# Optimization experiments

Measured on AMD Instinct MI355X. Metric: run time of the kernel, lower is better.

## Reference

```python
import jax, jax.numpy as jnp
import numpy as np

B = 8192
IN = 2048
H = 2048


def setup_inputs() -> dict:
    key = jax.random.key(0)
    ks = jax.random.split(key, 11)
    s_w = 1.0 / np.sqrt(IN + H)  # torch Linear default init scale
    inp = {
        "input": jax.random.normal(ks[0], (B, IN), jnp.float32),
        "h_prev": jax.random.normal(ks[1], (B, H), jnp.float32),
        "c_prev": jax.random.normal(ks[2], (B, H), jnp.float32),
        "Wf": jax.random.normal(ks[3], (H, IN + H), jnp.float32) * s_w,
        "bf": jax.random.normal(ks[4], (H,), jnp.float32) * s_w,
        "Wi": jax.random.normal(ks[5], (H, IN + H), jnp.float32) * s_w,
        "bi": jax.random.normal(ks[6], (H,), jnp.float32) * s_w,
        "Wg": jax.random.normal(ks[7], (H, IN + H), jnp.float32) * s_w,
        "bg": jax.random.normal(ks[8], (H,), jnp.float32) * s_w,
        "Wo": jax.random.normal(ks[9], (H, IN + H), jnp.float32) * s_w,
        "bo": jax.random.normal(ks[10], (H,), jnp.float32) * s_w,
    }
    return inp


def reference(input, h_prev, c_prev, Wf, bf, Wi, bi, Wg, bg, Wo, bo):
    # combined: [B, IN+H]
    combined = jnp.concatenate([input, h_prev], axis=1)
    # Fuse the 4 gate GEMMs into one: W_all [4H, IN+H]
    W_all = jnp.concatenate([Wf, Wi, Wg, Wo], axis=0)
    b_all = jnp.concatenate([bf, bi, bg, bo], axis=0)
    gates = combined @ W_all.T + b_all  # [B, 4H]
    f_, i_, g_, o_ = jnp.split(gates, 4, axis=1)
    f = jax.nn.sigmoid(f_)
    i = jax.nn.sigmoid(i_)
    g = jnp.tanh(g_)
    o = jax.nn.sigmoid(o_)
    c = f * c_prev + i * g
    h = o * jnp.tanh(c)
    return (h, c)
```

## Files before the change

kernel.cpp:

```cpp
#include <hip/hip_runtime.h>
#include <stdint.h>


#define BQ 8192
#define INF 2048
#define HH 2048
#define KK 4096

typedef __attribute__((ext_vector_type(8))) short short8;
typedef __attribute__((ext_vector_type(8))) unsigned short ushort8;
typedef __attribute__((ext_vector_type(4))) float floatx4;

__device__ __forceinline__ unsigned short f2b(float f) {
    unsigned u = __float_as_uint(f);
    u += 0x7fff + ((u >> 16) & 1);
    return (unsigned short)(u >> 16);
}
__device__ __forceinline__ ushort8 cvt8(float4 a, float4 b) {
    ushort8 y;
    y[0] = f2b(a.x); y[1] = f2b(a.y); y[2] = f2b(a.z); y[3] = f2b(a.w);
    y[4] = f2b(b.x); y[5] = f2b(b.y); y[6] = f2b(b.z); y[7] = f2b(b.w);
    return y;
}
__device__ __forceinline__ float fsig(float x) {
    return 1.f / (1.f + __expf(-x));
}
__device__ __forceinline__ float ftanh(float x) {
    return 1.f - 2.f / (__expf(2.f * x) + 1.f);
}

__global__ __launch_bounds__(256) void pack_all(
    const float4* __restrict__ inp, const float4* __restrict__ hp,
    const float4* __restrict__ w0, const float4* __restrict__ w1,
    const float4* __restrict__ w2, const float4* __restrict__ w3,
    unsigned short* __restrict__ comb, unsigned short* __restrict__ wpk)
{
    const int NC16 = BQ * INF / 16;
    int v = blockIdx.x * 256 + threadIdx.x;
    if (v < 2 * NC16) {
        int isH = v >= NC16;
        int u16 = v - (isH ? NC16 : 0);
        const float4* src = isH ? hp : inp;
        float4 x0 = src[u16 * 4];
        float4 x1 = src[u16 * 4 + 1];
        float4 x2 = src[u16 * 4 + 2];
        float4 x3 = src[u16 * 4 + 3];
        int u = u16 * 16;
        int b = u >> 11;
        int k = u & 2047;
        unsigned short* d = comb + (size_t)b * KK + k + (isH ? INF : 0);
        *(ushort8*)d       = cvt8(x0, x1);
        *(ushort8*)(d + 8) = cvt8(x2, x3);
    } else {
        int w = v - 2 * NC16;
        size_t e = (size_t)w * 16;
        int g = (int)(e >> 23);
        int u = (int)(e & ((1u << 23) - 1));
        int h = u >> 12;
        int k = u & 4095;
        const float4* src = (g == 0) ? w0 : (g == 1) ? w1 : (g == 2) ? w2 : w3;
        float4 x0 = src[(u >> 2)];
        float4 x1 = src[(u >> 2) + 1];
        float4 x2 = src[(u >> 2) + 2];
        float4 x3 = src[(u >> 2) + 3];
        int p = ((h >> 5) << 7) + (g << 5) + (h & 31);
        unsigned short* d = wpk + (size_t)p * KK + k;
        *(ushort8*)d       = cvt8(x0, x1);
        *(ushort8*)(d + 8) = cvt8(x2, x3);
    }
}

__global__ __launch_bounds__(512, 2) void lstm_fused(
    const unsigned short* __restrict__ A,
    const unsigned short* __restrict__ W,
    const float* __restrict__ cprev,
    const float* __restrict__ bf_, const float* __restrict__ bi_,
    const float* __restrict__ bg_, const float* __restrict__ bo_,
    float* __restrict__ out)
{
    __shared__ unsigned short lds[65536];
    char* ldsb = (char*)lds;

    const int t    = threadIdx.x;
    const int wv   = t >> 6;
    const int lane = t & 63;
    const int wm   = wv >> 1;
    const int wn   = wv & 1;
    const int fr   = lane & 15;
    const int fq   = lane >> 4;

    int lin = blockIdx.y * 32 + blockIdx.x;
    lin = (lin & 7) * 128 + (lin >> 3);
    const int m0 = (lin >> 5) << 8;
    const int n0 = (lin & 31) << 8;

    const int koff = ((lane & 7) ^ (lane >> 3)) << 3;
    const unsigned short* aR = A + (size_t)(m0 + wv * 16 + (lane >> 3)) * KK + koff;
    const unsigned short* bR = W + (size_t)(n0 + wv * 16 + (lane >> 3)) * KK + koff;
    const int stgOff = wv * 16 * 128;

    const int x7    = fr & 7;
    const int aBase = (wm >> 1) * 16384 + ((wm & 1) * 64 + fr) * 128;
    const int bBase = 32768 + wn * 16384 + fr * 128;

    floatx4 acc[4][8];
#pragma unroll
    for (int i = 0; i < 4; ++i)
#pragma unroll
        for (int j = 0; j < 8; ++j) acc[i][j] = (floatx4)0.f;

    short8 aA[4][2];
    short8 bb[2][2];

#define STAGE(srcbase, ldsoff, kk)                                              \
    do {                                                                        \
        __builtin_amdgcn_global_load_lds(                                       \
            (const __attribute__((address_space(1))) void*)((srcbase) + (kk)),  \
            (__attribute__((address_space(3))) void*)(ldsb + (ldsoff) + stgOff),\
            16, 0, 0);                                                          \
        __builtin_amdgcn_global_load_lds(                                       \
            (const __attribute__((address_space(1))) void*)((srcbase) + 8 * KK + (kk)), \
            (__attribute__((address_space(3))) void*)(ldsb + (ldsoff) + stgOff + 1024), \
            16, 0, 0);                                                          \
    } while (0)

    auto LDA = [&](int side, int i, short8* d) {
        const char* p = ldsb + side * 65536 + aBase + i * 2048;
        d[0] = *(const short8*)(p + ((fq ^ x7) << 4));
        d[1] = *(const short8*)(p + (((4 + fq) ^ x7) << 4));
    };
    auto LDB = [&](int side, int j, short8* d) {
        const char* p = ldsb + side * 65536 + bBase + j * 2048;
        d[0] = *(const short8*)(p + ((fq ^ x7) << 4));
        d[1] = *(const short8*)(p + (((4 + fq) ^ x7) << 4));
    };
    auto MM = [&](const short8* a, const short8* b, floatx4& c) {
        c = __builtin_amdgcn_mfma_f32_16x16x32_bf16(a[0], b[0], c, 0, 0, 0);
        c = __builtin_amdgcn_mfma_f32_16x16x32_bf16(a[1], b[1], c, 0, 0, 0);
    };

#define BAR()  __builtin_amdgcn_s_barrier()
#define SB0()  __builtin_amdgcn_sched_barrier(0)
#define VM4()  do { asm volatile("s_waitcnt vmcnt(4)" ::: "memory"); SB0(); } while (0)

#define CLUSTER(p)                                                    \
    do {                                                              \
        __builtin_amdgcn_s_setprio(1);                                \
        _Pragma("unroll")                                             \
        for (int i = 0; i < 4; ++i) {                                 \
            MM(aA[i], bb[0], acc[i][2 * (p)]);                        \
            MM(aA[i], bb[1], acc[i][2 * (p) + 1]);                    \
        }                                                             \
        __builtin_amdgcn_s_setprio(0);                                \
    } while (0)

    STAGE(aR, 0, 0);
    STAGE(aR + 128 * KK, 16384, 0);
    STAGE(bR, 32768, 0);
    STAGE(bR + 128 * KK, 49152, 0);
    STAGE(aR, 65536, 64);
    STAGE(aR + 128 * KK, 81920, 64);
    VM4();
    BAR();

#pragma unroll 1
    for (int it = 0; it < 32; ++it) {
        const int k1 = ((2 * it + 1) & 63) << 6;
        const int k2 = ((2 * it + 2) & 63) << 6;
        const int k3 = ((2 * it + 3) & 63) << 6;

        LDA(0, 0, aA[0]); LDB(0, 0, bb[0]); LDB(0, 1, bb[1]);
        LDA(0, 1, aA[1]); LDA(0, 2, aA[2]); LDA(0, 3, aA[3]);
        STAGE(bR, 98304, k1);
        SB0();
        CLUSTER(0);
        BAR();

        LDB(0, 2, bb[0]); LDB(0, 3, bb[1]);
        STAGE(bR + 128 * KK, 114688, k1);
        SB0();
        CLUSTER(1);
        BAR();

        LDB(0, 4, bb[0]); LDB(0, 5, bb[1]);
        STAGE(aR, 0, k2);
        SB0();
        CLUSTER(2);
        BAR();

        LDB(0, 6, bb[0]); LDB(0, 7, bb[1]);
        STAGE(aR + 128 * KK, 16384, k2);
        SB0();
        CLUSTER(3);
        VM4();
        BAR();

        LDA(1, 0, aA[0]); LDB(1, 0, bb[0]); LDB(1, 1, bb[1]);
        LDA(1, 1, aA[1]); LDA(1, 2, aA[2]); LDA(1, 3, aA[3]);
        STAGE(bR, 32768, k2);
        SB0();
        CLUSTER(0);
        BAR();

        LDB(1, 2, bb[0]); LDB(1, 3, bb[1]);
        STAGE(bR + 128 * KK, 49152, k2);
        SB0();
        CLUSTER(1);
        BAR();

        LDB(1, 4, bb[0]); LDB(1, 5, bb[1]);
        STAGE(aR, 65536, k3);
        SB0();
        CLUSTER(2);
        BAR();

        LDB(1, 6, bb[0]); LDB(1, 7, bb[1]);
        STAGE(aR + 128 * KK, 81920, k3);
        SB0();
        CLUSTER(3);
        VM4();
        BAR();
    }

    const int hb = (n0 >> 2) + wn * 32;
    float bF[2], bI[2], bG[2], bO[2];
#pragma unroll
    for (int jh = 0; jh < 2; ++jh) {
        int h = hb + jh * 16 + fr;
        bF[jh] = bf_[h]; bI[jh] = bi_[h]; bG[jh] = bg_[h]; bO[jh] = bo_[h];
    }
    const int rowb = m0 + wm * 64 + fq * 4;
#pragma unroll
    for (int i = 0; i < 4; ++i) {
#pragma unroll
        for (int r = 0; r < 4; ++r) {
            int row = rowb + i * 16 + r;
#pragma unroll
            for (int jh = 0; jh < 2; ++jh) {
                int h = hb + jh * 16 + fr;
                size_t gi = (size_t)row * HH + h;
                float xf = acc[i][0 + jh][r] + bF[jh];
                float xi = acc[i][2 + jh][r] + bI[jh];
                float xg = acc[i][4 + jh][r] + bG[jh];
                float xo = acc[i][6 + jh][r] + bO[jh];
                float f  = fsig(xf);
                float ii = fsig(xi);
                float g  = ftanh(xg);
                float o  = fsig(xo);
                float c  = f * cprev[gi] + ii * g;
                float hv = o * ftanh(c);
                out[gi] = hv;
                out[(size_t)BQ * HH + gi] = c;
            }
        }
    }
}

extern "C" void kernel_launch(void* const* d_in, const int* in_sizes, int n_in,
                              void* d_out, int out_size, void* d_ws, size_t ws_size,
                              hipStream_t stream) {
    const float* input  = (const float*)d_in[0];
    const float* h_prev = (const float*)d_in[1];
    const float* c_prev = (const float*)d_in[2];
    const float* Wf = (const float*)d_in[3];
    const float* bf_ = (const float*)d_in[4];
    const float* Wi = (const float*)d_in[5];
    const float* bi_ = (const float*)d_in[6];
    const float* Wg = (const float*)d_in[7];
    const float* bg_ = (const float*)d_in[8];
    const float* Wo = (const float*)d_in[9];
    const float* bo_ = (const float*)d_in[10];
    float* out = (float*)d_out;

    unsigned short* combined = (unsigned short*)d_ws;
    unsigned short* Wpk = (unsigned short*)d_ws + (size_t)BQ * KK;

    pack_all<<<dim3(16384), 256, 0, stream>>>(
        (const float4*)input, (const float4*)h_prev,
        (const float4*)Wf, (const float4*)Wi, (const float4*)Wg, (const float4*)Wo,
        combined, Wpk);
    lstm_fused<<<dim3(32, 32), 512, 0, stream>>>(
        combined, Wpk, c_prev, bf_, bi_, bg_, bo_, out);
}
```

Baseline: 797.1 us.

## Switch to 32x32x16 MFMA tiles and prefetch A/B fragments across phases

Replaces the 16x16x32 bf16 MFMA with 32x32x16 bf16 MFMA, so each wave holds 2x4 floatx16 accumulators instead of 4x8 floatx4. Fewer, larger MFMAs need fewer LDS fragment reads per FLOP. The LDS read schedule is also rebuilt: B fragments are double-buffered in registers (bbA/bbB) and the next A tile is loaded at the end of the previous half-iteration. The vmcnt wait moves earlier and is tightened to vmcnt(2). The epilogue is remapped to the 32x32 output layout, and register pressure changes with the new fragment arrays.

Measured after the change: 2.379 ms. 198% more time.

```diff
diff --git a/kernel.cpp b/kernel.cpp
--- a/kernel.cpp
+++ b/kernel.cpp
@@ -9,7 +9,7 @@
 
 typedef __attribute__((ext_vector_type(8))) short short8;
 typedef __attribute__((ext_vector_type(8))) unsigned short ushort8;
-typedef __attribute__((ext_vector_type(4))) float floatx4;
+typedef __attribute__((ext_vector_type(16))) float floatx16;
 
 __device__ __forceinline__ unsigned short f2b(float f) {
     unsigned u = __float_as_uint(f);
@@ -86,8 +86,9 @@
     const int lane = t & 63;
     const int wm   = wv >> 1;
     const int wn   = wv & 1;
-    const int fr   = lane & 15;
-    const int fq   = lane >> 4;
+    const int lq   = lane & 31;
+    const int lh   = lane >> 5;
+    const int x7   = lq & 7;
 
     int lin = blockIdx.y * 32 + blockIdx.x;
     lin = (lin & 7) * 128 + (lin >> 3);
@@ -99,18 +100,20 @@
     const unsigned short* bR = W + (size_t)(n0 + wv * 16 + (lane >> 3)) * KK + koff;
     const int stgOff = wv * 16 * 128;
 
-    const int x7    = fr & 7;
-    const int aBase = (wm >> 1) * 16384 + ((wm & 1) * 64 + fr) * 128;
-    const int bBase = 32768 + wn * 16384 + fr * 128;
-
-    floatx4 acc[4][8];
-#pragma unroll
-    for (int i = 0; i < 4; ++i)
-#pragma unroll
-        for (int j = 0; j < 8; ++j) acc[i][j] = (floatx4)0.f;
-
-    short8 aA[4][2];
-    short8 bb[2][2];
+    const int aRow = (wm >> 1) * 16384 + (((wm & 1) * 64 + lq) * 128);
+    const int bRow = 32768 + wn * 16384 + lq * 128;
+    int gOff[4];
+#pragma unroll
+    for (int ks = 0; ks < 4; ++ks) gOff[ks] = ((2 * ks + lh) ^ x7) << 4;
+
+    floatx16 acc[2][4];
+#pragma unroll
+    for (int i = 0; i < 2; ++i)
+#pragma unroll
+        for (int g = 0; g < 4; ++g) acc[i][g] = (floatx16)0.f;
+
+    short8 aF[2][4];
+    short8 bbA[4], bbB[4];
 
 #define STAGE(srcbase, ldsoff, kk)                                              \
     do {                                                                        \
@@ -124,34 +127,35 @@
             16, 0, 0);                                                          \
     } while (0)
 
-    auto LDA = [&](int side, int i, short8* d) {
-        const char* p = ldsb + side * 65536 + aBase + i * 2048;
-        d[0] = *(const short8*)(p + ((fq ^ x7) << 4));
-        d[1] = *(const short8*)(p + (((4 + fq) ^ x7) << 4));
+    auto LDAall = [&](int side) {
+#pragma unroll
+        for (int i = 0; i < 2; ++i)
+#pragma unroll
+            for (int ks = 0; ks < 4; ++ks)
+                aF[i][ks] = *(const short8*)(ldsb + side * 65536 + aRow + i * 4096 + gOff[ks]);
     };
-    auto LDB = [&](int side, int j, short8* d) {
-        const char* p = ldsb + side * 65536 + bBase + j * 2048;
-        d[0] = *(const short8*)(p + ((fq ^ x7) << 4));
-        d[1] = *(const short8*)(p + (((4 + fq) ^ x7) << 4));
-    };
-    auto MM = [&](const short8* a, const short8* b, floatx4& c) {
-        c = __builtin_amdgcn_mfma_f32_16x16x32_bf16(a[0], b[0], c, 0, 0, 0);
-        c = __builtin_amdgcn_mfma_f32_16x16x32_bf16(a[1], b[1], c, 0, 0, 0);
+    auto LDB = [&](int side, int g, short8* d) {
+#pragma unroll
+        for (int ks = 0; ks < 4; ++ks)
+            d[ks] = *(const short8*)(ldsb + side * 65536 + bRow + g * 4096 + gOff[ks]);
     };
 
 #define BAR()  __builtin_amdgcn_s_barrier()
 #define SB0()  __builtin_amdgcn_sched_barrier(0)
+#define VM2()  do { asm volatile("s_waitcnt vmcnt(2)" ::: "memory"); SB0(); } while (0)
 #define VM4()  do { asm volatile("s_waitcnt vmcnt(4)" ::: "memory"); SB0(); } while (0)
 
-#define CLUSTER(p)                                                    \
-    do {                                                              \
-        __builtin_amdgcn_s_setprio(1);                                \
-        _Pragma("unroll")                                             \
-        for (int i = 0; i < 4; ++i) {                                 \
-            MM(aA[i], bb[0], acc[i][2 * (p)]);                        \
-            MM(aA[i], bb[1], acc[i][2 * (p) + 1]);                    \
-        }                                                             \
-        __builtin_amdgcn_s_setprio(0);                                \
+#define CL(g, Bb)                                                              \
+    do {                                                                       \
+        __builtin_amdgcn_s_setprio(1);                                         \
+        _Pragma("unroll")                                                      \
+        for (int ks = 0; ks < 4; ++ks) {                                       \
+            acc[0][g] = __builtin_amdgcn_mfma_f32_32x32x16_bf16(               \
+                aF[0][ks], Bb[ks], acc[0][g], 0, 0, 0);                        \
+            acc[1][g] = __builtin_amdgcn_mfma_f32_32x32x16_bf16(               \
+                aF[1][ks], Bb[ks], acc[1][g], 0, 0, 0);                        \
+        }                                                                      \
+        __builtin_amdgcn_s_setprio(0);                                         \
     } while (0)
 
     STAGE(aR, 0, 0);
@@ -162,6 +166,9 @@
     STAGE(aR + 128 * KK, 81920, 64);
     VM4();
     BAR();
+    SB0();
+    LDAall(0);
+    LDB(0, 0, bbA);
 
 #pragma unroll 1
     for (int it = 0; it < 32; ++it) {
@@ -169,89 +176,82 @@
         const int k2 = ((2 * it + 2) & 63) << 6;
         const int k3 = ((2 * it + 3) & 63) << 6;
 
-        LDA(0, 0, aA[0]); LDB(0, 0, bb[0]); LDB(0, 1, bb[1]);
-        LDA(0, 1, aA[1]); LDA(0, 2, aA[2]); LDA(0, 3, aA[3]);
+        LDB(0, 1, bbB);
         STAGE(bR, 98304, k1);
         SB0();
-        CLUSTER(0);
-        BAR();
-
-        LDB(0, 2, bb[0]); LDB(0, 3, bb[1]);
+        CL(0, bbA);
+        BAR();
+
+        LDB(0, 2, bbA);
         STAGE(bR + 128 * KK, 114688, k1);
         SB0();
-        CLUSTER(1);
-        BAR();
-
-        LDB(0, 4, bb[0]); LDB(0, 5, bb[1]);
+        CL(1, bbB);
+        BAR();
+
+        LDB(0, 3, bbB);
         STAGE(aR, 0, k2);
         SB0();
-        CLUSTER(2);
-        BAR();
-
-        LDB(0, 6, bb[0]); LDB(0, 7, bb[1]);
+        CL(2, bbA);
+        VM2();
+        BAR();
+        SB0();
+
+        LDB(1, 0, bbA);
         STAGE(aR + 128 * KK, 16384, k2);
         SB0();
-        CLUSTER(3);
-        VM4();
-        BAR();
-
-        LDA(1, 0, aA[0]); LDB(1, 0, bb[0]); LDB(1, 1, bb[1]);
-        LDA(1, 1, aA[1]); LDA(1, 2, aA[2]); LDA(1, 3, aA[3]);
+        CL(3, bbB);
+        LDAall(1);
+        BAR();
+
+        LDB(1, 1, bbB);
         STAGE(bR, 32768, k2);
         SB0();
-        CLUSTER(0);
-        BAR();
-
-        LDB(1, 2, bb[0]); LDB(1, 3, bb[1]);
+        CL(0, bbA);
+        BAR();
+
+        LDB(1, 2, bbA);
         STAGE(bR + 128 * KK, 49152, k2);
         SB0();
-        CLUSTER(1);
-        BAR();
-
-        LDB(1, 4, bb[0]); LDB(1, 5, bb[1]);
+        CL(1, bbB);
+        BAR();
+
+        LDB(1, 3, bbB);
         STAGE(aR, 65536, k3);
         SB0();
-        CLUSTER(2);
-        BAR();
-
-        LDB(1, 6, bb[0]); LDB(1, 7, bb[1]);
+        CL(2, bbA);
+        VM2();
+        BAR();
+        SB0();
+
+        LDB(0, 0, bbA);
         STAGE(aR + 128 * KK, 81920, k3);
         SB0();
-        CLUSTER(3);
-        VM4();
+        CL(3, bbB);
+        LDAall(0);
         BAR();
     }
 
-    const int hb = (n0 >> 2) + wn * 32;
-    float bF[2], bI[2], bG[2], bO[2];
-#pragma unroll
-    for (int jh = 0; jh < 2; ++jh) {
-        int h = hb + jh * 16 + fr;
-        bF[jh] = bf_[h]; bI[jh] = bi_[h]; bG[jh] = bg_[h]; bO[jh] = bo_[h];
-    }
-    const int rowb = m0 + wm * 64 + fq * 4;
-#pragma unroll
-    for (int i = 0; i < 4; ++i) {
-#pragma unroll
-        for (int r = 0; r < 4; ++r) {
-            int row = rowb + i * 16 + r;
-#pragma unroll
-            for (int jh = 0; jh < 2; ++jh) {
-                int h = hb + jh * 16 + fr;
-                size_t gi = (size_t)row * HH + h;
-                float xf = acc[i][0 + jh][r] + bF[jh];
-                float xi = acc[i][2 + jh][r] + bI[jh];
-                float xg = acc[i][4 + jh][r] + bG[jh];
-                float xo = acc[i][6 + jh][r] + bO[jh];
-                float f  = fsig(xf);
-                float ii = fsig(xi);
-                float g  = ftanh(xg);
-                float o  = fsig(xo);
-                float c  = f * cprev[gi] + ii * g;
-                float hv = o * ftanh(c);
-                out[gi] = hv;
-                out[(size_t)BQ * HH + gi] = c;
-            }
+    const int h = (n0 >> 2) + wn * 32 + lq;
+    const float bFv = bf_[h], bIv = bi_[h], bGv = bg_[h], bOv = bo_[h];
+    const int rowb = m0 + wm * 64 + 4 * lh;
+#pragma unroll
+    for (int i = 0; i < 2; ++i) {
+#pragma unroll
+        for (int reg = 0; reg < 16; ++reg) {
+            int row = rowb + i * 32 + (reg & 3) + 8 * (reg >> 2);
+            size_t gi = (size_t)row * HH + h;
+            float xf = acc[i][0][reg] + bFv;
+            float xi = acc[i][1][reg] + bIv;
+            float xg = acc[i][2][reg] + bGv;
+            float xo = acc[i][3][reg] + bOv;
+            float f  = fsig(xf);
+            float ii = fsig(xi);
+            float g  = ftanh(xg);
+            float o  = fsig(xo);
+            float c  = f * cprev[gi] + ii * g;
+            float hv = o * ftanh(c);
+            out[gi] = hv;
+            out[(size_t)BQ * HH + gi] = c;
         }
     }
 }
```
